# Kernel tuning notes

Hardware: AMD Instinct MI355X
Metric: run time of the kernel (lower is better)

The kernel has to match this reference:

```python
import jax, jax.numpy as jnp
import numpy as np

B, S, D, DOUT, E = 2, 2048, 1024, 1024, 8
DH = 4 * D  # expert hidden size


def setup_inputs() -> dict:
    key = jax.random.key(0)
    ks = jax.random.split(key, 7)
    sc = lambda *sh: 1.0 / np.sqrt(sh[-2]) if len(sh) >= 2 else 0.02
    return {
        "x": jax.random.normal(ks[0], (B, S, D), jnp.float32),
        "Wg": jax.random.normal(ks[1], (D, E), jnp.float32) / np.sqrt(D),
        "bg": jnp.zeros((E,), jnp.float32),
        "W1": jax.random.normal(ks[2], (E, D, DH), jnp.float32) / np.sqrt(D),
        "b1": jax.random.normal(ks[3], (E, DH), jnp.float32) * 0.02,
        "W2": jax.random.normal(ks[4], (E, DH, DOUT), jnp.float32) / np.sqrt(DH),
        "b2": jax.random.normal(ks[5], (E, DOUT), jnp.float32) * 0.02,
    }


def reference(x, Wg, bg, W1, b1, W2, b2):
    # x: [B, S, D] -> flatten tokens (chunking over seq in the original is
    # math-neutral: routing and expert MLP are per-token).
    Bb, Ss, Dd = x.shape
    xt = x.reshape(-1, Dd)                       # [T, D]
    # Gate: softmax then argmax (top-1 routing, output NOT scaled by gate prob)
    gates = jax.nn.softmax(xt @ Wg + bg, axis=-1)  # [T, E]
    sel = jnp.argmax(gates, axis=-1)               # [T]
    nE = W1.shape[0]
    out = jnp.zeros((xt.shape[0], W2.shape[-1]), x.dtype)
    # Grouped expert MLP expressed as masked dense loop over the small fixed
    # expert count (jit-friendly; a fused gather-grouped-GEMM-scatter kernel
    # is the optimization target).
    for e in range(nE):
        h = jax.nn.gelu(xt @ W1[e] + b1[e], approximate=False)  # [T, 4D]
        ye = h @ W2[e] + b2[e]                                  # [T, DOUT]
        out = jnp.where((sel == e)[:, None], ye, out)
    return out.reshape(Bb, Ss, -1)
```

## Files before the change

kernel.cpp:

```cpp
#include <hip/hip_runtime.h>
#include <hip/hip_bf16.h>
#include <math.h>

#define T_TOK 4096
#define DIM   1024
#define NEXP  8
#define DHID  4096
#define NDOUT 1024
#define BM    128
#define BN    128
#define BK    64
#define MAXTILES 40

typedef short bf16x8 __attribute__((ext_vector_type(8)));
typedef float f32x4 __attribute__((ext_vector_type(4)));

__device__ __forceinline__ unsigned short f2bf(float f) {
  unsigned u = __float_as_uint(f);
  u += 0x7fffu + ((u >> 16) & 1u);
  return (unsigned short)(u >> 16);
}
__device__ __forceinline__ unsigned pack2bf(float a, float b) {
  return (unsigned)f2bf(a) | ((unsigned)f2bf(b) << 16);
}
__device__ __forceinline__ void gl_lds16(const void* g, void* l) {
  __builtin_amdgcn_global_load_lds(
      (const __attribute__((address_space(1))) void*)g,
      (__attribute__((address_space(3))) void*)l, 16, 0, 0);
}

__global__ __launch_bounds__(256)
void gate_kernel(const float* __restrict__ x, const float* __restrict__ Wg,
                 const float* __restrict__ bg, int* __restrict__ sel) {
  int lane = threadIdx.x & 63;
  int wid  = threadIdx.x >> 6;
  int t = blockIdx.x * 4 + wid;
  if (t >= T_TOK) return;
  const float* xr = x + (size_t)t * DIM;
  double acc[NEXP];
#pragma unroll
  for (int e = 0; e < NEXP; e++) acc[e] = 0.0;
  for (int j = 0; j < DIM / 64; j++) {
    int d = lane + j * 64;
    float xv = xr[d];
    const float4* wr = reinterpret_cast<const float4*>(Wg + (size_t)d * NEXP);
    float4 w0 = wr[0], w1 = wr[1];
    acc[0] += (double)xv * (double)w0.x;
    acc[1] += (double)xv * (double)w0.y;
    acc[2] += (double)xv * (double)w0.z;
    acc[3] += (double)xv * (double)w0.w;
    acc[4] += (double)xv * (double)w1.x;
    acc[5] += (double)xv * (double)w1.y;
    acc[6] += (double)xv * (double)w1.z;
    acc[7] += (double)xv * (double)w1.w;
  }
#pragma unroll
  for (int off = 32; off >= 1; off >>= 1) {
#pragma unroll
    for (int e = 0; e < NEXP; e++) acc[e] += __shfl_down(acc[e], off);
  }
  if (lane == 0) {
    double best = acc[0] + (double)bg[0];
    int bi = 0;
#pragma unroll
    for (int e = 1; e < NEXP; e++) {
      double v = acc[e] + (double)bg[e];
      if (v > best) { best = v; bi = e; }
    }
    sel[t] = bi;
  }
}

__global__ void zero_kernel(int* __restrict__ counts) {
  if (threadIdx.x < NEXP) counts[threadIdx.x] = 0;
}

__global__ void hist_kernel(const int* __restrict__ sel, int* __restrict__ counts) {
  __shared__ int lc[NEXP];
  if (threadIdx.x < NEXP) lc[threadIdx.x] = 0;
  __syncthreads();
  int t = blockIdx.x * 256 + threadIdx.x;
  atomicAdd(&lc[sel[t]], 1);
  __syncthreads();
  if (threadIdx.x < NEXP) atomicAdd(&counts[threadIdx.x], lc[threadIdx.x]);
}

__global__ void plan_kernel(const int* __restrict__ counts, int* __restrict__ base,
                            int* __restrict__ cursor, int* __restrict__ tileExpert,
                            int* __restrict__ tilePos, int* __restrict__ tileRows,
                            int* __restrict__ ntiles) {
  if (threadIdx.x == 0) {
    int acc = 0, nt = 0;
    for (int e = 0; e < NEXP; e++) {
      base[e] = acc; cursor[e] = acc;
      int c = counts[e];
      for (int j = 0; j < c; j += BM) {
        tileExpert[nt] = e;
        tilePos[nt]    = acc + j;
        int rem = c - j;
        tileRows[nt]   = rem < BM ? rem : BM;
        nt++;
      }
      acc += c;
    }
    *ntiles = nt;
  }
}

__global__ void scatter_kernel(const int* __restrict__ sel, int* __restrict__ cursor,
                               int* __restrict__ list) {
  __shared__ int lcnt[NEXP];
  __shared__ int lbase[NEXP];
  int tid = threadIdx.x;
  if (tid < NEXP) lcnt[tid] = 0;
  __syncthreads();
  int t = blockIdx.x * 256 + tid;
  int e = sel[t];
  int lpos = atomicAdd(&lcnt[e], 1);
  __syncthreads();
  if (tid < NEXP) lbase[tid] = atomicAdd(&cursor[tid], lcnt[tid]);
  __syncthreads();
  list[lbase[e] + lpos] = t;
}

__global__ __launch_bounds__(256)
void convert_x_kernel(const float* __restrict__ x, unsigned short* __restrict__ xbf) {
  int i = (blockIdx.x * 256 + threadIdx.x) * 8;
  float4 a = *(const float4*)(x + i);
  float4 b = *(const float4*)(x + i + 4);
  uint4 o;
  o.x = pack2bf(a.x, a.y); o.y = pack2bf(a.z, a.w);
  o.z = pack2bf(b.x, b.y); o.w = pack2bf(b.z, b.w);
  *(uint4*)(xbf + i) = o;
}

__global__ __launch_bounds__(256)
void transpose_convert_kernel(const float* __restrict__ in, unsigned short* __restrict__ out,
                              int K, int N) {
  int nb = blockIdx.x, kb = blockIdx.y, e = blockIdx.z;
  const float* inp = in + (size_t)e * K * N;
  unsigned short* outp = out + (size_t)e * N * K;
  __shared__ unsigned short lds[64][72];
  int tx = threadIdx.x;
  int kloc = tx >> 4;
  int n4   = (tx & 15) << 2;
#pragma unroll
  for (int p = 0; p < 4; p++) {
    int k = p * 16 + kloc;
    float4 v = *(const float4*)(inp + (size_t)(kb * 64 + k) * N + nb * 64 + n4);
    lds[n4 + 0][k] = f2bf(v.x);
    lds[n4 + 1][k] = f2bf(v.y);
    lds[n4 + 2][k] = f2bf(v.z);
    lds[n4 + 3][k] = f2bf(v.w);
  }
  __syncthreads();
  int n  = tx >> 2;
  int kq = (tx & 3) << 4;
  uint4 a = *(const uint4*)&lds[n][kq];
  uint4 b = *(const uint4*)&lds[n][kq + 8];
  unsigned short* o = outp + (size_t)(nb * 64 + n) * K + kb * 64 + kq;
  *(uint4*)o = a;
  *(uint4*)(o + 8) = b;
}

__global__ __launch_bounds__(256)
void gemm1_kernel(const unsigned short* __restrict__ xbf, const unsigned short* __restrict__ W1T,
                  const float* __restrict__ b1, const int* __restrict__ list,
                  const int* __restrict__ tileExpert, const int* __restrict__ tilePos,
                  const int* __restrict__ tileRows, const int* __restrict__ ntiles,
                  unsigned short* __restrict__ Hc) {
  int tIdx = blockIdx.x;
  if (tIdx >= *ntiles) return;
  int e       = tileExpert[tIdx];
  int posBase = tilePos[tIdx];
  int rows    = tileRows[tIdx];
  int n0      = blockIdx.y * BN;

  __shared__ __align__(1024) unsigned char As[2][BM * 128];
  __shared__ __align__(1024) unsigned char Bs[2][BN * 128];

  const int tx   = threadIdx.x;
  const int lane = tx & 63;
  const int w    = tx >> 6;
  const int wm = w >> 1, wn = w & 1;
  const int u    = lane & 7;
  const int rsub = lane >> 3;
  const int px   = (u ^ rsub) << 4;

  const char* aSrc[4];
  const char* bSrc[4];
#pragma unroll
  for (int l = 0; l < 4; l++) {
    int r = w * 32 + l * 8 + rsub;
    int tok = list[posBase + (r < rows ? r : 0)];
    aSrc[l] = (const char*)xbf + ((size_t)tok * DIM) * 2 + px;
    bSrc[l] = (const char*)W1T + (((size_t)e * DHID + n0 + r) * DIM) * 2 + px;
  }

  f32x4 acc[4][4];
#pragma unroll
  for (int mf = 0; mf < 4; mf++)
#pragma unroll
    for (int nf = 0; nf < 4; nf++)
      acc[mf][nf] = f32x4{0.f, 0.f, 0.f, 0.f};

  const int NT = DIM / BK;
  auto stage = [&](int buf, int kt) {
    int kb = kt * 128;
#pragma unroll
    for (int l = 0; l < 4; l++) {
      gl_lds16(aSrc[l] + kb, &As[buf][(w * 32 + l * 8) * 128]);
      gl_lds16(bSrc[l] + kb, &Bs[buf][(w * 32 + l * 8) * 128]);
    }
  };
  auto compute = [&](int buf) {
#pragma unroll
    for (int ks = 0; ks < 2; ks++) {
      int kbl = ks * 64 + (lane >> 4) * 16;
      bf16x8 af[4], bv[4];
#pragma unroll
      for (int mf = 0; mf < 4; mf++) {
        int row = (wm << 6) + (mf << 4) + (lane & 15);
        af[mf] = *(const bf16x8*)&As[buf][row * 128 + (kbl ^ ((row & 7) << 4))];
      }
#pragma unroll
      for (int nf = 0; nf < 4; nf++) {
        int row = (wn << 6) + (nf << 4) + (lane & 15);
        bv[nf] = *(const bf16x8*)&Bs[buf][row * 128 + (kbl ^ ((row & 7) << 4))];
      }
#pragma unroll
      for (int mf = 0; mf < 4; mf++)
#pragma unroll
        for (int nf = 0; nf < 4; nf++)
          acc[mf][nf] = __builtin_amdgcn_mfma_f32_16x16x32_bf16(af[mf], bv[nf], acc[mf][nf], 0, 0, 0);
    }
  };

  stage(0, 0);
  __syncthreads();
  int cur = 0;
  for (int kt = 0; kt < NT; kt++) {
    if (kt + 1 < NT) stage(cur ^ 1, kt + 1);
    compute(cur);
    __syncthreads();
    cur ^= 1;
  }

  const float* b1e = b1 + (size_t)e * DHID;
#pragma unroll
  for (int nf = 0; nf < 4; nf++) {
    int col = n0 + (wn << 6) + (nf << 4) + (lane & 15);
    float bias = b1e[col];
#pragma unroll
    for (int mf = 0; mf < 4; mf++) {
#pragma unroll
      for (int j = 0; j < 4; j++) {
        int rloc = (wm << 6) + (mf << 4) + ((lane >> 4) << 2) + j;
        if (rloc < rows) {
          float h = acc[mf][nf][j] + bias;
          float g = 0.5f * h * (1.0f + erff(h * 0.70710678118654752f));
          Hc[(size_t)(posBase + rloc) * DHID + col] = f2bf(g);
        }
      }
    }
  }
}

__global__ __launch_bounds__(256)
void gemm2_kernel(const unsigned short* __restrict__ Hc, const unsigned short* __restrict__ W2T,
                  const float* __restrict__ b2, const int* __restrict__ list,
                  const int* __restrict__ tileExpert, const int* __restrict__ tilePos,
                  const int* __restrict__ tileRows, const int* __restrict__ ntiles,
                  float* __restrict__ out) {
  int tIdx = blockIdx.x;
  if (tIdx >= *ntiles) return;
  int e       = tileExpert[tIdx];
  int posBase = tilePos[tIdx];
  int rows    = tileRows[tIdx];
  int n0      = blockIdx.y * BN;

  __shared__ __align__(1024) unsigned char As[2][BM * 128];
  __shared__ __align__(1024) unsigned char Bs[2][BN * 128];

  const int tx   = threadIdx.x;
  const int lane = tx & 63;
  const int w    = tx >> 6;
  const int wm = w >> 1, wn = w & 1;
  const int u    = lane & 7;
  const int rsub = lane >> 3;
  const int px   = (u ^ rsub) << 4;

  const char* aSrc[4];
  const char* bSrc[4];
#pragma unroll
  for (int l = 0; l < 4; l++) {
    int r = w * 32 + l * 8 + rsub;
    int ar = posBase + (r < rows ? r : 0);
    aSrc[l] = (const char*)Hc + ((size_t)ar * DHID) * 2 + px;
    bSrc[l] = (const char*)W2T + (((size_t)e * NDOUT + n0 + r) * DHID) * 2 + px;
  }

  f32x4 acc[4][4];
#pragma unroll
  for (int mf = 0; mf < 4; mf++)
#pragma unroll
    for (int nf = 0; nf < 4; nf++)
      acc[mf][nf] = f32x4{0.f, 0.f, 0.f, 0.f};

  const int NT = DHID / BK;
  auto stage = [&](int buf, int kt) {
    int kb = kt * 128;
#pragma unroll
    for (int l = 0; l < 4; l++) {
      gl_lds16(aSrc[l] + kb, &As[buf][(w * 32 + l * 8) * 128]);
      gl_lds16(bSrc[l] + kb, &Bs[buf][(w * 32 + l * 8) * 128]);
    }
  };
  auto compute = [&](int buf) {
#pragma unroll
    for (int ks = 0; ks < 2; ks++) {
      int kbl = ks * 64 + (lane >> 4) * 16;
      bf16x8 af[4], bv[4];
#pragma unroll
      for (int mf = 0; mf < 4; mf++) {
        int row = (wm << 6) + (mf << 4) + (lane & 15);
        af[mf] = *(const bf16x8*)&As[buf][row * 128 + (kbl ^ ((row & 7) << 4))];
      }
#pragma unroll
      for (int nf = 0; nf < 4; nf++) {
        int row = (wn << 6) + (nf << 4) + (lane & 15);
        bv[nf] = *(const bf16x8*)&Bs[buf][row * 128 + (kbl ^ ((row & 7) << 4))];
      }
#pragma unroll
      for (int mf = 0; mf < 4; mf++)
#pragma unroll
        for (int nf = 0; nf < 4; nf++)
          acc[mf][nf] = __builtin_amdgcn_mfma_f32_16x16x32_bf16(af[mf], bv[nf], acc[mf][nf], 0, 0, 0);
    }
  };

  stage(0, 0);
  __syncthreads();
  int cur = 0;
  for (int kt = 0; kt < NT; kt++) {
    if (kt + 1 < NT) stage(cur ^ 1, kt + 1);
    compute(cur);
    __syncthreads();
    cur ^= 1;
  }

  const float* b2e = b2 + (size_t)e * NDOUT;
  int trow[4][4];
#pragma unroll
  for (int mf = 0; mf < 4; mf++)
#pragma unroll
    for (int j = 0; j < 4; j++) {
      int rloc = (wm << 6) + (mf << 4) + ((lane >> 4) << 2) + j;
      trow[mf][j] = (rloc < rows) ? list[posBase + rloc] : -1;
    }
#pragma unroll
  for (int nf = 0; nf < 4; nf++) {
    int col = n0 + (wn << 6) + (nf << 4) + (lane & 15);
    float bias = b2e[col];
#pragma unroll
    for (int mf = 0; mf < 4; mf++)
#pragma unroll
      for (int j = 0; j < 4; j++) {
        int t = trow[mf][j];
        if (t >= 0) out[(size_t)t * NDOUT + col] = acc[mf][nf][j] + bias;
      }
  }
}

extern "C" void kernel_launch(void* const* d_in, const int* in_sizes, int n_in,
                              void* d_out, int out_size, void* d_ws, size_t ws_size,
                              hipStream_t stream) {
  const float* x  = (const float*)d_in[0];
  const float* Wg = (const float*)d_in[1];
  const float* bg = (const float*)d_in[2];
  const float* W1 = (const float*)d_in[3];
  const float* b1 = (const float*)d_in[4];
  const float* W2 = (const float*)d_in[5];
  const float* b2 = (const float*)d_in[6];
  float* out = (float*)d_out;

  char* ws = (char*)d_ws;
  int* sel        = (int*)(ws);
  int* counts     = (int*)(ws + 16384);
  int* base       = (int*)(ws + 16448);
  int* cursor     = (int*)(ws + 16512);
  int* ntiles     = (int*)(ws + 16576);
  int* tileExpert = (int*)(ws + 16640);
  int* tilePos    = (int*)(ws + 16832);
  int* tileRows   = (int*)(ws + 17024);
  int* list       = (int*)(ws + 17408);

  unsigned short* xbf = (unsigned short*)(ws + (1ull << 20));
  unsigned short* Hc  = (unsigned short*)(ws + (16ull << 20));
  unsigned short* W1T = (unsigned short*)(ws + (48ull << 20));
  unsigned short* W2T = (unsigned short*)(ws + (112ull << 20));

  gate_kernel<<<T_TOK / 4, 256, 0, stream>>>(x, Wg, bg, sel);
  zero_kernel<<<1, 64, 0, stream>>>(counts);
  hist_kernel<<<T_TOK / 256, 256, 0, stream>>>(sel, counts);
  plan_kernel<<<1, 64, 0, stream>>>(counts, base, cursor, tileExpert, tilePos, tileRows, ntiles);
  scatter_kernel<<<T_TOK / 256, 256, 0, stream>>>(sel, cursor, list);

  convert_x_kernel<<<T_TOK * DIM / (256 * 8), 256, 0, stream>>>(x, xbf);
  transpose_convert_kernel<<<dim3(DHID / 64, DIM / 64, NEXP), 256, 0, stream>>>(W1, W1T, DIM, DHID);
  transpose_convert_kernel<<<dim3(NDOUT / 64, DHID / 64, NEXP), 256, 0, stream>>>(W2, W2T, DHID, NDOUT);

  gemm1_kernel<<<dim3(MAXTILES, DHID / BN), 256, 0, stream>>>(
      xbf, W1T, b1, list, tileExpert, tilePos, tileRows, ntiles, Hc);
  gemm2_kernel<<<dim3(MAXTILES, NDOUT / BN), 256, 0, stream>>>(
      Hc, W2T, b2, list, tileExpert, tilePos, tileRows, ntiles, out);
}
```

Measured before the change: 320.5 us.

## Use 256x256 tiles with staged pipelined MFMA schedule and split-K expert GEMM2

Both expert GEMMs move from 128x128 tiles with 256 threads to 256x256 tiles with 512 threads and a 128KB LDS double buffer. Each k-step is split into quarter-tile phases that interleave LDS reads, async global-to-LDS loads, explicit vmcnt waits, barriers and priority-raised MFMA bursts. The aim is more data reuse per tile and better overlap of memory traffic with matrix math. GEMM2 is split along K into two halves that write fp32 partials into workspace reused from the W1T region, and a new reduce kernel sums the halves and scatters rows back to token order. This adds an extra 32MB partial write and read plus one more launch, and with 256-row tiles the last tile of each expert carries more padding.

```diff
diff --git a/kernel.cpp b/kernel.cpp
--- a/kernel.cpp
+++ b/kernel.cpp
@@ -7,10 +7,7 @@
 #define NEXP  8
 #define DHID  4096
 #define NDOUT 1024
-#define BM    128
-#define BN    128
-#define BK    64
-#define MAXTILES 40
+#define MAXT2 24
 
 typedef short bf16x8 __attribute__((ext_vector_type(8)));
 typedef float f32x4 __attribute__((ext_vector_type(4)));
@@ -28,6 +25,8 @@
       (const __attribute__((address_space(1))) void*)g,
       (__attribute__((address_space(3))) void*)l, 16, 0, 0);
 }
+#define SBAR()  __builtin_amdgcn_s_barrier()
+#define SCHED() __builtin_amdgcn_sched_barrier(0)
 
 __global__ __launch_bounds__(256)
 void gate_kernel(const float* __restrict__ x, const float* __restrict__ Wg,
@@ -94,11 +93,11 @@
     for (int e = 0; e < NEXP; e++) {
       base[e] = acc; cursor[e] = acc;
       int c = counts[e];
-      for (int j = 0; j < c; j += BM) {
+      for (int j = 0; j < c; j += 256) {
         tileExpert[nt] = e;
         tilePos[nt]    = acc + j;
         int rem = c - j;
-        tileRows[nt]   = rem < BM ? rem : BM;
+        tileRows[nt]   = rem < 256 ? rem : 256;
         nt++;
       }
       acc += c;
@@ -163,213 +162,297 @@
   *(uint4*)(o + 8) = b;
 }
 
-__global__ __launch_bounds__(256)
+
+__global__ __launch_bounds__(512)
 void gemm1_kernel(const unsigned short* __restrict__ xbf, const unsigned short* __restrict__ W1T,
                   const float* __restrict__ b1, const int* __restrict__ list,
                   const int* __restrict__ tileExpert, const int* __restrict__ tilePos,
                   const int* __restrict__ tileRows, const int* __restrict__ ntiles,
                   unsigned short* __restrict__ Hc) {
-  int tIdx = blockIdx.x;
+  int tIdx = blockIdx.y;
   if (tIdx >= *ntiles) return;
-  int e       = tileExpert[tIdx];
-  int posBase = tilePos[tIdx];
-  int rows    = tileRows[tIdx];
-  int n0      = blockIdx.y * BN;
-
-  __shared__ __align__(1024) unsigned char As[2][BM * 128];
-  __shared__ __align__(1024) unsigned char Bs[2][BN * 128];
-
-  const int tx   = threadIdx.x;
-  const int lane = tx & 63;
-  const int w    = tx >> 6;
-  const int wm = w >> 1, wn = w & 1;
-  const int u    = lane & 7;
+  int e = tileExpert[tIdx], posBase = tilePos[tIdx], rows = tileRows[tIdx];
+  int n0 = blockIdx.x * 256;
+
+  __shared__ __align__(1024) char LDS[131072];
+
+  const int tx = threadIdx.x, lane = tx & 63, w = tx >> 6;
+  const int wm = w >> 2, wn = w & 3;
   const int rsub = lane >> 3;
-  const int px   = (u ^ rsub) << 4;
-
-  const char* aSrc[4];
-  const char* bSrc[4];
-#pragma unroll
-  for (int l = 0; l < 4; l++) {
-    int r = w * 32 + l * 8 + rsub;
-    int tok = list[posBase + (r < rows ? r : 0)];
-    aSrc[l] = (const char*)xbf + ((size_t)tok * DIM) * 2 + px;
-    bSrc[l] = (const char*)W1T + (((size_t)e * DHID + n0 + r) * DIM) * 2 + px;
-  }
-
-  f32x4 acc[4][4];
-#pragma unroll
-  for (int mf = 0; mf < 4; mf++)
-#pragma unroll
-    for (int nf = 0; nf < 4; nf++)
-      acc[mf][nf] = f32x4{0.f, 0.f, 0.f, 0.f};
-
-  const int NT = DIM / BK;
-  auto stage = [&](int buf, int kt) {
-    int kb = kt * 128;
-#pragma unroll
-    for (int l = 0; l < 4; l++) {
-      gl_lds16(aSrc[l] + kb, &As[buf][(w * 32 + l * 8) * 128]);
-      gl_lds16(bSrc[l] + kb, &Bs[buf][(w * 32 + l * 8) * 128]);
-    }
-  };
-  auto compute = [&](int buf) {
-#pragma unroll
-    for (int ks = 0; ks < 2; ks++) {
-      int kbl = ks * 64 + (lane >> 4) * 16;
-      bf16x8 af[4], bv[4];
-#pragma unroll
-      for (int mf = 0; mf < 4; mf++) {
-        int row = (wm << 6) + (mf << 4) + (lane & 15);
-        af[mf] = *(const bf16x8*)&As[buf][row * 128 + (kbl ^ ((row & 7) << 4))];
+  const int px = ((lane & 7) ^ rsub) << 4;
+
+  const char* aS[2][2];
+  const char* bS[2][2];
+#pragma unroll
+  for (int h = 0; h < 2; h++)
+#pragma unroll
+    for (int j = 0; j < 2; j++) {
+      int rl = w * 16 + j * 8 + rsub;
+      int ar = h * 128 + rl; if (ar >= rows) ar = rows - 1;
+      int tok = list[posBase + ar];
+      aS[h][j] = (const char*)xbf + (size_t)tok * (DIM * 2) + px;
+      bS[h][j] = (const char*)W1T + ((size_t)e * DHID + n0 + h * 128 + rl) * (DIM * 2) + px;
+    }
+
+  auto STAGE = [&](int buf, int isB, int half, int kt) {
+    char* base = &LDS[((buf * 2 + isB) * 2 + half) * 16384 + w * 2048];
+    const char* s0 = (isB ? bS[half][0] : aS[half][0]) + kt * 128;
+    const char* s1 = (isB ? bS[half][1] : aS[half][1]) + kt * 128;
+    gl_lds16(s0, base);
+    gl_lds16(s1, base + 1024);
+  };
+
+  const int koff0 = ((lane >> 4) * 16) ^ ((lane & 7) << 4);
+  const int koff1 = (64 + (lane >> 4) * 16) ^ ((lane & 7) << 4);
+
+  bf16x8 aF[4][2], bF0[2][2], bF1[2][2];
+  f32x4 acc[2][2][4][2];
+#pragma unroll
+  for (int qm = 0; qm < 2; qm++)
+#pragma unroll
+    for (int qn = 0; qn < 2; qn++)
+#pragma unroll
+      for (int mf = 0; mf < 4; mf++)
+#pragma unroll
+        for (int nf = 0; nf < 2; nf++)
+          acc[qm][qn][mf][nf] = f32x4{0.f, 0.f, 0.f, 0.f};
+
+  auto RDA = [&](int buf, int qm) {
+    const char* Ab = &LDS[((buf * 2 + 0) * 2 + qm) * 16384];
+#pragma unroll
+    for (int mf = 0; mf < 4; mf++) {
+      int ro = (wm * 64 + mf * 16 + (lane & 15)) * 128;
+      aF[mf][0] = *(const bf16x8*)(Ab + ro + koff0);
+      aF[mf][1] = *(const bf16x8*)(Ab + ro + koff1);
+    }
+  };
+  auto RDB = [&](int buf, int qn, bf16x8 (&bF)[2][2]) {
+    const char* Bb = &LDS[((buf * 2 + 1) * 2 + qn) * 16384];
+#pragma unroll
+    for (int nf = 0; nf < 2; nf++) {
+      int ro = (wn * 32 + nf * 16 + (lane & 15)) * 128;
+      bF[nf][0] = *(const bf16x8*)(Bb + ro + koff0);
+      bF[nf][1] = *(const bf16x8*)(Bb + ro + koff1);
+    }
+  };
+  auto MFMA16 = [&](int qm, int qn, bf16x8 (&bF)[2][2]) {
+    __builtin_amdgcn_s_setprio(1);
+#pragma unroll
+    for (int mf = 0; mf < 4; mf++)
+#pragma unroll
+      for (int nf = 0; nf < 2; nf++) {
+        acc[qm][qn][mf][nf] = __builtin_amdgcn_mfma_f32_16x16x32_bf16(aF[mf][0], bF[nf][0], acc[qm][qn][mf][nf], 0, 0, 0);
+        acc[qm][qn][mf][nf] = __builtin_amdgcn_mfma_f32_16x16x32_bf16(aF[mf][1], bF[nf][1], acc[qm][qn][mf][nf], 0, 0, 0);
       }
-#pragma unroll
-      for (int nf = 0; nf < 4; nf++) {
-        int row = (wn << 6) + (nf << 4) + (lane & 15);
-        bv[nf] = *(const bf16x8*)&Bs[buf][row * 128 + (kbl ^ ((row & 7) << 4))];
+    __builtin_amdgcn_s_setprio(0);
+  };
+
+  const int NTt = DIM / 64;
+  STAGE(0, 0, 0, 0); STAGE(0, 1, 0, 0); STAGE(0, 1, 1, 0); STAGE(0, 0, 1, 0);
+  STAGE(1, 0, 0, 1); STAGE(1, 1, 0, 1);
+  asm volatile("s_waitcnt vmcnt(4)" ::: "memory");
+  SCHED(); SBAR(); SCHED();
+
+  for (int T = 0; T < NTt; T++) {
+    int buf = T & 1, nbuf = buf ^ 1;
+    RDA(buf, 0); RDB(buf, 0, bF0);
+    if (T + 1 < NTt) STAGE(nbuf, 1, 1, T + 1);
+    SCHED(); SBAR(); SCHED();
+    MFMA16(0, 0, bF0);
+    SCHED(); SBAR(); SCHED();
+    RDB(buf, 1, bF1);
+    if (T + 1 < NTt) STAGE(nbuf, 0, 1, T + 1);
+    SCHED(); SBAR(); SCHED();
+    MFMA16(0, 1, bF1);
+    SCHED(); SBAR(); SCHED();
+    RDA(buf, 1);
+    if (T + 2 < NTt) STAGE(buf, 0, 0, T + 2);
+    SCHED(); SBAR(); SCHED();
+    MFMA16(1, 1, bF1);
+    SCHED(); SBAR(); SCHED();
+    if (T + 2 < NTt) {
+      STAGE(buf, 1, 0, T + 2);
+      asm volatile("s_waitcnt vmcnt(4)" ::: "memory");
+    } else if (T + 1 < NTt) {
+      asm volatile("s_waitcnt vmcnt(0)" ::: "memory");
+    }
+    SCHED(); SBAR(); SCHED();
+    MFMA16(1, 0, bF0);
+    SCHED(); SBAR(); SCHED();
+  }
+
+  const float* b1e = b1 + (size_t)e * DHID;
+#pragma unroll
+  for (int qm = 0; qm < 2; qm++)
+#pragma unroll
+    for (int qn = 0; qn < 2; qn++)
+#pragma unroll
+      for (int nf = 0; nf < 2; nf++) {
+        int col = n0 + qn * 128 + wn * 32 + nf * 16 + (lane & 15);
+        float bias = b1e[col];
+#pragma unroll
+        for (int mf = 0; mf < 4; mf++)
+#pragma unroll
+          for (int j = 0; j < 4; j++) {
+            int rloc = qm * 128 + wm * 64 + mf * 16 + ((lane >> 4) << 2) + j;
+            if (rloc < rows) {
+              float h = acc[qm][qn][mf][nf][j] + bias;
+              float g = 0.5f * h * (1.0f + erff(h * 0.70710678118654752f));
+              Hc[(size_t)(posBase + rloc) * DHID + col] = f2bf(g);
+            }
+          }
       }
+}
+
+__global__ __launch_bounds__(512)
+void gemm2_kernel(const unsigned short* __restrict__ Hc, const unsigned short* __restrict__ W2T,
+                  const float* __restrict__ b2, const int* __restrict__ tileExpert,
+                  const int* __restrict__ tilePos, const int* __restrict__ tileRows,
+                  const int* __restrict__ ntiles, float* __restrict__ Ppart) {
+  int tIdx = blockIdx.y;
+  if (tIdx >= *ntiles) return;
+  int e = tileExpert[tIdx], posBase = tilePos[tIdx], rows = tileRows[tIdx];
+  int n0 = blockIdx.x * 256;
+  int zs = blockIdx.z;
+  int kt0 = zs * 32;
+
+  __shared__ __align__(1024) char LDS[131072];
+
+  const int tx = threadIdx.x, lane = tx & 63, w = tx >> 6;
+  const int wm = w >> 2, wn = w & 3;
+  const int rsub = lane >> 3;
+  const int px = ((lane & 7) ^ rsub) << 4;
+
+  const char* aS[2][2];
+  const char* bS[2][2];
+#pragma unroll
+  for (int h = 0; h < 2; h++)
+#pragma unroll
+    for (int j = 0; j < 2; j++) {
+      int rl = w * 16 + j * 8 + rsub;
+      int ar = h * 128 + rl; if (ar >= rows) ar = rows - 1;
+      aS[h][j] = (const char*)Hc + (size_t)(posBase + ar) * (DHID * 2) + (size_t)kt0 * 128 + px;
+      bS[h][j] = (const char*)W2T + ((size_t)e * NDOUT + n0 + h * 128 + rl) * (DHID * 2) + (size_t)kt0 * 128 + px;
+    }
+
+  auto STAGE = [&](int buf, int isB, int half, int kt) {
+    char* base = &LDS[((buf * 2 + isB) * 2 + half) * 16384 + w * 2048];
+    const char* s0 = (isB ? bS[half][0] : aS[half][0]) + kt * 128;
+    const char* s1 = (isB ? bS[half][1] : aS[half][1]) + kt * 128;
+    gl_lds16(s0, base);
+    gl_lds16(s1, base + 1024);
+  };
+
+  const int koff0 = ((lane >> 4) * 16) ^ ((lane & 7) << 4);
+  const int koff1 = (64 + (lane >> 4) * 16) ^ ((lane & 7) << 4);
+
+  bf16x8 aF[4][2], bF0[2][2], bF1[2][2];
+  f32x4 acc[2][2][4][2];
+#pragma unroll
+  for (int qm = 0; qm < 2; qm++)
+#pragma unroll
+    for (int qn = 0; qn < 2; qn++)
 #pragma unroll
       for (int mf = 0; mf < 4; mf++)
 #pragma unroll
-        for (int nf = 0; nf < 4; nf++)
-          acc[mf][nf] = __builtin_amdgcn_mfma_f32_16x16x32_bf16(af[mf], bv[nf], acc[mf][nf], 0, 0, 0);
-    }
-  };
-
-  stage(0, 0);
-  __syncthreads();
-  int cur = 0;
-  for (int kt = 0; kt < NT; kt++) {
-    if (kt + 1 < NT) stage(cur ^ 1, kt + 1);
-    compute(cur);
-    __syncthreads();
-    cur ^= 1;
-  }
-
-  const float* b1e = b1 + (size_t)e * DHID;
-#pragma unroll
-  for (int nf = 0; nf < 4; nf++) {
-    int col = n0 + (wn << 6) + (nf << 4) + (lane & 15);
-    float bias = b1e[col];
+        for (int nf = 0; nf < 2; nf++)
+          acc[qm][qn][mf][nf] = f32x4{0.f, 0.f, 0.f, 0.f};
+
+  auto RDA = [&](int buf, int qm) {
+    const char* Ab = &LDS[((buf * 2 + 0) * 2 + qm) * 16384];
 #pragma unroll
     for (int mf = 0; mf < 4; mf++) {
-#pragma unroll
-      for (int j = 0; j < 4; j++) {
-        int rloc = (wm << 6) + (mf << 4) + ((lane >> 4) << 2) + j;
-        if (rloc < rows) {
-          float h = acc[mf][nf][j] + bias;
-          float g = 0.5f * h * (1.0f + erff(h * 0.70710678118654752f));
-          Hc[(size_t)(posBase + rloc) * DHID + col] = f2bf(g);
-        }
+      int ro = (wm * 64 + mf * 16 + (lane & 15)) * 128;
+      aF[mf][0] = *(const bf16x8*)(Ab + ro + koff0);
+      aF[mf][1] = *(const bf16x8*)(Ab + ro + koff1);
+    }
+  };
+  auto RDB = [&](int buf, int qn, bf16x8 (&bF)[2][2]) {
+    const char* Bb = &LDS[((buf * 2 + 1) * 2 + qn) * 16384];
+#pragma unroll
+    for (int nf = 0; nf < 2; nf++) {
+      int ro = (wn * 32 + nf * 16 + (lane & 15)) * 128;
+      bF[nf][0] = *(const bf16x8*)(Bb + ro + koff0);
+      bF[nf][1] = *(const bf16x8*)(Bb + ro + koff1);
+    }
+  };
+  auto MFMA16 = [&](int qm, int qn, bf16x8 (&bF)[2][2]) {
+    __builtin_amdgcn_s_setprio(1);
+#pragma unroll
+    for (int mf = 0; mf < 4; mf++)
+#pragma unroll
+      for (int nf = 0; nf < 2; nf++) {
+        acc[qm][qn][mf][nf] = __builtin_amdgcn_mfma_f32_16x16x32_bf16(aF[mf][0], bF[nf][0], acc[qm][qn][mf][nf], 0, 0, 0);
+        acc[qm][qn][mf][nf] = __builtin_amdgcn_mfma_f32_16x16x32_bf16(aF[mf][1], bF[nf][1], acc[qm][qn][mf][nf], 0, 0, 0);
       }
-    }
-  }
+    __builtin_amdgcn_s_setprio(0);
+  };
+
+  const int NTt = 32;
+  STAGE(0, 0, 0, 0); STAGE(0, 1, 0, 0); STAGE(0, 1, 1, 0); STAGE(0, 0, 1, 0);
+  STAGE(1, 0, 0, 1); STAGE(1, 1, 0, 1);
+  asm volatile("s_waitcnt vmcnt(4)" ::: "memory");
+  SCHED(); SBAR(); SCHED();
+
+  for (int T = 0; T < NTt; T++) {
+    int buf = T & 1, nbuf = buf ^ 1;
+    RDA(buf, 0); RDB(buf, 0, bF0);
+    if (T + 1 < NTt) STAGE(nbuf, 1, 1, T + 1);
+    SCHED(); SBAR(); SCHED();
+    MFMA16(0, 0, bF0);
+    SCHED(); SBAR(); SCHED();
+    RDB(buf, 1, bF1);
+    if (T + 1 < NTt) STAGE(nbuf, 0, 1, T + 1);
+    SCHED(); SBAR(); SCHED();
+    MFMA16(0, 1, bF1);
+    SCHED(); SBAR(); SCHED();
+    RDA(buf, 1);
+    if (T + 2 < NTt) STAGE(buf, 0, 0, T + 2);
+    SCHED(); SBAR(); SCHED();
+    MFMA16(1, 1, bF1);
+    SCHED(); SBAR(); SCHED();
+    if (T + 2 < NTt) {
+      STAGE(buf, 1, 0, T + 2);
+      asm volatile("s_waitcnt vmcnt(4)" ::: "memory");
+    } else if (T + 1 < NTt) {
+      asm volatile("s_waitcnt vmcnt(0)" ::: "memory");
+    }
+    SCHED(); SBAR(); SCHED();
+    MFMA16(1, 0, bF0);
+    SCHED(); SBAR(); SCHED();
+  }
+
+  const float* b2e = b2 + (size_t)e * NDOUT;
+  float* P = Ppart + (size_t)zs * T_TOK * NDOUT;
+#pragma unroll
+  for (int qm = 0; qm < 2; qm++)
+#pragma unroll
+    for (int qn = 0; qn < 2; qn++)
+#pragma unroll
+      for (int nf = 0; nf < 2; nf++) {
+        int col = n0 + qn * 128 + wn * 32 + nf * 16 + (lane & 15);
+        float bias = (zs == 0) ? b2e[col] : 0.f;
+#pragma unroll
+        for (int mf = 0; mf < 4; mf++)
+#pragma unroll
+          for (int j = 0; j < 4; j++) {
+            int rloc = qm * 128 + wm * 64 + mf * 16 + ((lane >> 4) << 2) + j;
+            if (rloc < rows)
+              P[(size_t)(posBase + rloc) * NDOUT + col] = acc[qm][qn][mf][nf][j] + bias;
+          }
+      }
 }
 
 __global__ __launch_bounds__(256)
-void gemm2_kernel(const unsigned short* __restrict__ Hc, const unsigned short* __restrict__ W2T,
-                  const float* __restrict__ b2, const int* __restrict__ list,
-                  const int* __restrict__ tileExpert, const int* __restrict__ tilePos,
-                  const int* __restrict__ tileRows, const int* __restrict__ ntiles,
-                  float* __restrict__ out) {
-  int tIdx = blockIdx.x;
-  if (tIdx >= *ntiles) return;
-  int e       = tileExpert[tIdx];
-  int posBase = tilePos[tIdx];
-  int rows    = tileRows[tIdx];
-  int n0      = blockIdx.y * BN;
-
-  __shared__ __align__(1024) unsigned char As[2][BM * 128];
-  __shared__ __align__(1024) unsigned char Bs[2][BN * 128];
-
-  const int tx   = threadIdx.x;
-  const int lane = tx & 63;
-  const int w    = tx >> 6;
-  const int wm = w >> 1, wn = w & 1;
-  const int u    = lane & 7;
-  const int rsub = lane >> 3;
-  const int px   = (u ^ rsub) << 4;
-
-  const char* aSrc[4];
-  const char* bSrc[4];
-#pragma unroll
-  for (int l = 0; l < 4; l++) {
-    int r = w * 32 + l * 8 + rsub;
-    int ar = posBase + (r < rows ? r : 0);
-    aSrc[l] = (const char*)Hc + ((size_t)ar * DHID) * 2 + px;
-    bSrc[l] = (const char*)W2T + (((size_t)e * NDOUT + n0 + r) * DHID) * 2 + px;
-  }
-
-  f32x4 acc[4][4];
-#pragma unroll
-  for (int mf = 0; mf < 4; mf++)
-#pragma unroll
-    for (int nf = 0; nf < 4; nf++)
-      acc[mf][nf] = f32x4{0.f, 0.f, 0.f, 0.f};
-
-  const int NT = DHID / BK;
-  auto stage = [&](int buf, int kt) {
-    int kb = kt * 128;
-#pragma unroll
-    for (int l = 0; l < 4; l++) {
-      gl_lds16(aSrc[l] + kb, &As[buf][(w * 32 + l * 8) * 128]);
-      gl_lds16(bSrc[l] + kb, &Bs[buf][(w * 32 + l * 8) * 128]);
-    }
-  };
-  auto compute = [&](int buf) {
-#pragma unroll
-    for (int ks = 0; ks < 2; ks++) {
-      int kbl = ks * 64 + (lane >> 4) * 16;
-      bf16x8 af[4], bv[4];
-#pragma unroll
-      for (int mf = 0; mf < 4; mf++) {
-        int row = (wm << 6) + (mf << 4) + (lane & 15);
-        af[mf] = *(const bf16x8*)&As[buf][row * 128 + (kbl ^ ((row & 7) << 4))];
-      }
-#pragma unroll
-      for (int nf = 0; nf < 4; nf++) {
-        int row = (wn << 6) + (nf << 4) + (lane & 15);
-        bv[nf] = *(const bf16x8*)&Bs[buf][row * 128 + (kbl ^ ((row & 7) << 4))];
-      }
-#pragma unroll
-      for (int mf = 0; mf < 4; mf++)
-#pragma unroll
-        for (int nf = 0; nf < 4; nf++)
-          acc[mf][nf] = __builtin_amdgcn_mfma_f32_16x16x32_bf16(af[mf], bv[nf], acc[mf][nf], 0, 0, 0);
-    }
-  };
-
-  stage(0, 0);
-  __syncthreads();
-  int cur = 0;
-  for (int kt = 0; kt < NT; kt++) {
-    if (kt + 1 < NT) stage(cur ^ 1, kt + 1);
-    compute(cur);
-    __syncthreads();
-    cur ^= 1;
-  }
-
-  const float* b2e = b2 + (size_t)e * NDOUT;
-  int trow[4][4];
-#pragma unroll
-  for (int mf = 0; mf < 4; mf++)
-#pragma unroll
-    for (int j = 0; j < 4; j++) {
-      int rloc = (wm << 6) + (mf << 4) + ((lane >> 4) << 2) + j;
-      trow[mf][j] = (rloc < rows) ? list[posBase + rloc] : -1;
-    }
-#pragma unroll
-  for (int nf = 0; nf < 4; nf++) {
-    int col = n0 + (wn << 6) + (nf << 4) + (lane & 15);
-    float bias = b2e[col];
-#pragma unroll
-    for (int mf = 0; mf < 4; mf++)
-#pragma unroll
-      for (int j = 0; j < 4; j++) {
-        int t = trow[mf][j];
-        if (t >= 0) out[(size_t)t * NDOUT + col] = acc[mf][nf][j] + bias;
-      }
-  }
+void reduce_kernel(const float* __restrict__ Ppart, const int* __restrict__ list,
+                   float* __restrict__ out) {
+  int pos = blockIdx.x;
+  int tok = list[pos];
+  int c = threadIdx.x * 4;
+  float4 a = *(const float4*)(Ppart + (size_t)pos * NDOUT + c);
+  float4 b = *(const float4*)(Ppart + (size_t)T_TOK * NDOUT + (size_t)pos * NDOUT + c);
+  float4 o; o.x = a.x + b.x; o.y = a.y + b.y; o.z = a.z + b.z; o.w = a.w + b.w;
+  *(float4*)(out + (size_t)tok * NDOUT + c) = o;
 }
 
 extern "C" void kernel_launch(void* const* d_in, const int* in_sizes, int n_in,
@@ -399,6 +482,7 @@
   unsigned short* Hc  = (unsigned short*)(ws + (16ull << 20));
   unsigned short* W1T = (unsigned short*)(ws + (48ull << 20));
   unsigned short* W2T = (unsigned short*)(ws + (112ull << 20));
+  float* Ppart        = (float*)(ws + (48ull << 20));
 
   gate_kernel<<<T_TOK / 4, 256, 0, stream>>>(x, Wg, bg, sel);
   zero_kernel<<<1, 64, 0, stream>>>(counts);
@@ -410,8 +494,9 @@
   transpose_convert_kernel<<<dim3(DHID / 64, DIM / 64, NEXP), 256, 0, stream>>>(W1, W1T, DIM, DHID);
   transpose_convert_kernel<<<dim3(NDOUT / 64, DHID / 64, NEXP), 256, 0, stream>>>(W2, W2T, DHID, NDOUT);
 
-  gemm1_kernel<<<dim3(MAXTILES, DHID / BN), 256, 0, stream>>>(
+  gemm1_kernel<<<dim3(DHID / 256, MAXT2), 512, 0, stream>>>(
       xbf, W1T, b1, list, tileExpert, tilePos, tileRows, ntiles, Hc);
-  gemm2_kernel<<<dim3(MAXTILES, NDOUT / BN), 256, 0, stream>>>(
-      Hc, W2T, b2, list, tileExpert, tilePos, tileRows, ntiles, out);
-}
+  gemm2_kernel<<<dim3(NDOUT / 256, MAXT2, 2), 512, 0, stream>>>(
+      Hc, W2T, b2, tileExpert, tilePos, tileRows, ntiles, Ppart);
+  reduce_kernel<<<T_TOK, 256, 0, stream>>>(Ppart, list, out);
+}
```

Result: faster. 289.5 us (-9.7%).

## Split-K the second expert GEMM, single-buffer LDS, and reorder grid axes

Applied to the files above, without the earlier changes.

The second grouped GEMM now splits its 4096-long K dimension in two along grid z. Each half writes fp32 partial results in compacted token order to a scratch buffer that reuses the W1T region. A new reduce kernel adds the two halves and scatters each row to its token position. Both GEMMs drop double-buffered LDS staging in favour of a single buffer synchronised twice per K step, which halves shared memory per block, and the grid axes are swapped so the N tile index varies fastest. The aim is more blocks in flight for the small-N second GEMM and higher occupancy, at the cost of an extra fp32 round trip through memory, an extra launch, and loss of load/compute overlap inside each block.

```diff
diff --git a/kernel.cpp b/kernel.cpp
--- a/kernel.cpp
+++ b/kernel.cpp
@@ -8,8 +8,6 @@
 #define DHID  4096
 #define NDOUT 1024
 #define BM    128
-#define BN    128
-#define BK    64
 #define MAXTILES 40
 
 typedef short bf16x8 __attribute__((ext_vector_type(8)));
@@ -163,38 +161,34 @@
   *(uint4*)(o + 8) = b;
 }
 
+
 __global__ __launch_bounds__(256)
 void gemm1_kernel(const unsigned short* __restrict__ xbf, const unsigned short* __restrict__ W1T,
                   const float* __restrict__ b1, const int* __restrict__ list,
                   const int* __restrict__ tileExpert, const int* __restrict__ tilePos,
                   const int* __restrict__ tileRows, const int* __restrict__ ntiles,
                   unsigned short* __restrict__ Hc) {
-  int tIdx = blockIdx.x;
+  int tIdx = blockIdx.y;
   if (tIdx >= *ntiles) return;
-  int e       = tileExpert[tIdx];
-  int posBase = tilePos[tIdx];
-  int rows    = tileRows[tIdx];
-  int n0      = blockIdx.y * BN;
-
-  __shared__ __align__(1024) unsigned char As[2][BM * 128];
-  __shared__ __align__(1024) unsigned char Bs[2][BN * 128];
-
-  const int tx   = threadIdx.x;
-  const int lane = tx & 63;
-  const int w    = tx >> 6;
+  int e = tileExpert[tIdx], posBase = tilePos[tIdx], rows = tileRows[tIdx];
+  int n0 = blockIdx.x * 128;
+
+  __shared__ __align__(1024) char As[128 * 128];
+  __shared__ __align__(1024) char Bs[128 * 128];
+
+  const int tx = threadIdx.x, lane = tx & 63, w = tx >> 6;
   const int wm = w >> 1, wn = w & 1;
-  const int u    = lane & 7;
   const int rsub = lane >> 3;
-  const int px   = (u ^ rsub) << 4;
-
-  const char* aSrc[4];
-  const char* bSrc[4];
-#pragma unroll
-  for (int l = 0; l < 4; l++) {
-    int r = w * 32 + l * 8 + rsub;
-    int tok = list[posBase + (r < rows ? r : 0)];
-    aSrc[l] = (const char*)xbf + ((size_t)tok * DIM) * 2 + px;
-    bSrc[l] = (const char*)W1T + (((size_t)e * DHID + n0 + r) * DIM) * 2 + px;
+  const int px = ((lane & 7) ^ rsub) << 4;
+
+  const char* aS[4];
+  const char* bS[4];
+#pragma unroll
+  for (int j = 0; j < 4; j++) {
+    int r = w * 32 + j * 8 + rsub;
+    int tok = list[posBase + (r < rows ? r : rows - 1)];
+    aS[j] = (const char*)xbf + (size_t)tok * (DIM * 2) + px;
+    bS[j] = (const char*)W1T + ((size_t)e * DHID + n0 + r) * (DIM * 2) + px;
   }
 
   f32x4 acc[4][4];
@@ -204,58 +198,44 @@
     for (int nf = 0; nf < 4; nf++)
       acc[mf][nf] = f32x4{0.f, 0.f, 0.f, 0.f};
 
-  const int NT = DIM / BK;
-  auto stage = [&](int buf, int kt) {
+  const int NT = DIM / 64;
+  for (int kt = 0; kt < NT; kt++) {
     int kb = kt * 128;
 #pragma unroll
-    for (int l = 0; l < 4; l++) {
-      gl_lds16(aSrc[l] + kb, &As[buf][(w * 32 + l * 8) * 128]);
-      gl_lds16(bSrc[l] + kb, &Bs[buf][(w * 32 + l * 8) * 128]);
-    }
-  };
-  auto compute = [&](int buf) {
+    for (int j = 0; j < 4; j++) {
+      gl_lds16(aS[j] + kb, &As[(w * 32 + j * 8) * 128]);
+      gl_lds16(bS[j] + kb, &Bs[(w * 32 + j * 8) * 128]);
+    }
+    __syncthreads();
 #pragma unroll
     for (int ks = 0; ks < 2; ks++) {
-      int kbl = ks * 64 + (lane >> 4) * 16;
-      bf16x8 af[4], bv[4];
-#pragma unroll
-      for (int mf = 0; mf < 4; mf++) {
-        int row = (wm << 6) + (mf << 4) + (lane & 15);
-        af[mf] = *(const bf16x8*)&As[buf][row * 128 + (kbl ^ ((row & 7) << 4))];
-      }
-#pragma unroll
-      for (int nf = 0; nf < 4; nf++) {
-        int row = (wn << 6) + (nf << 4) + (lane & 15);
-        bv[nf] = *(const bf16x8*)&Bs[buf][row * 128 + (kbl ^ ((row & 7) << 4))];
-      }
+      int koff = (ks * 64 + (lane >> 4) * 16) ^ ((lane & 7) << 4);
+      bf16x8 aF[4], bF[4];
 #pragma unroll
       for (int mf = 0; mf < 4; mf++)
+        aF[mf] = *(const bf16x8*)&As[(wm * 64 + mf * 16 + (lane & 15)) * 128 + koff];
+#pragma unroll
+      for (int nf = 0; nf < 4; nf++)
+        bF[nf] = *(const bf16x8*)&Bs[(wn * 64 + nf * 16 + (lane & 15)) * 128 + koff];
+#pragma unroll
+      for (int mf = 0; mf < 4; mf++)
 #pragma unroll
         for (int nf = 0; nf < 4; nf++)
-          acc[mf][nf] = __builtin_amdgcn_mfma_f32_16x16x32_bf16(af[mf], bv[nf], acc[mf][nf], 0, 0, 0);
-    }
-  };
-
-  stage(0, 0);
-  __syncthreads();
-  int cur = 0;
-  for (int kt = 0; kt < NT; kt++) {
-    if (kt + 1 < NT) stage(cur ^ 1, kt + 1);
-    compute(cur);
+          acc[mf][nf] = __builtin_amdgcn_mfma_f32_16x16x32_bf16(aF[mf], bF[nf], acc[mf][nf], 0, 0, 0);
+    }
     __syncthreads();
-    cur ^= 1;
   }
 
   const float* b1e = b1 + (size_t)e * DHID;
 #pragma unroll
   for (int nf = 0; nf < 4; nf++) {
-    int col = n0 + (wn << 6) + (nf << 4) + (lane & 15);
+    int col = n0 + wn * 64 + nf * 16 + (lane & 15);
     float bias = b1e[col];
 #pragma unroll
     for (int mf = 0; mf < 4; mf++) {
 #pragma unroll
       for (int j = 0; j < 4; j++) {
-        int rloc = (wm << 6) + (mf << 4) + ((lane >> 4) << 2) + j;
+        int rloc = wm * 64 + mf * 16 + ((lane >> 4) << 2) + j;
         if (rloc < rows) {
           float h = acc[mf][nf][j] + bias;
           float g = 0.5f * h * (1.0f + erff(h * 0.70710678118654752f));
@@ -268,36 +248,32 @@
 
 __global__ __launch_bounds__(256)
 void gemm2_kernel(const unsigned short* __restrict__ Hc, const unsigned short* __restrict__ W2T,
-                  const float* __restrict__ b2, const int* __restrict__ list,
-                  const int* __restrict__ tileExpert, const int* __restrict__ tilePos,
-                  const int* __restrict__ tileRows, const int* __restrict__ ntiles,
-                  float* __restrict__ out) {
-  int tIdx = blockIdx.x;
+                  const float* __restrict__ b2, const int* __restrict__ tileExpert,
+                  const int* __restrict__ tilePos, const int* __restrict__ tileRows,
+                  const int* __restrict__ ntiles, float* __restrict__ Ppart) {
+  int tIdx = blockIdx.y;
   if (tIdx >= *ntiles) return;
-  int e       = tileExpert[tIdx];
-  int posBase = tilePos[tIdx];
-  int rows    = tileRows[tIdx];
-  int n0      = blockIdx.y * BN;
-
-  __shared__ __align__(1024) unsigned char As[2][BM * 128];
-  __shared__ __align__(1024) unsigned char Bs[2][BN * 128];
-
-  const int tx   = threadIdx.x;
-  const int lane = tx & 63;
-  const int w    = tx >> 6;
+  int e = tileExpert[tIdx], posBase = tilePos[tIdx], rows = tileRows[tIdx];
+  int n0 = blockIdx.x * 128;
+  int zs = blockIdx.z;
+  size_t kbyte0 = (size_t)zs * 32 * 128;
+
+  __shared__ __align__(1024) char As[128 * 128];
+  __shared__ __align__(1024) char Bs[128 * 128];
+
+  const int tx = threadIdx.x, lane = tx & 63, w = tx >> 6;
   const int wm = w >> 1, wn = w & 1;
-  const int u    = lane & 7;
   const int rsub = lane >> 3;
-  const int px   = (u ^ rsub) << 4;
-
-  const char* aSrc[4];
-  const char* bSrc[4];
-#pragma unroll
-  for (int l = 0; l < 4; l++) {
-    int r = w * 32 + l * 8 + rsub;
-    int ar = posBase + (r < rows ? r : 0);
-    aSrc[l] = (const char*)Hc + ((size_t)ar * DHID) * 2 + px;
-    bSrc[l] = (const char*)W2T + (((size_t)e * NDOUT + n0 + r) * DHID) * 2 + px;
+  const int px = ((lane & 7) ^ rsub) << 4;
+
+  const char* aS[4];
+  const char* bS[4];
+#pragma unroll
+  for (int j = 0; j < 4; j++) {
+    int r = w * 32 + j * 8 + rsub;
+    int ar = posBase + (r < rows ? r : rows - 1);
+    aS[j] = (const char*)Hc + (size_t)ar * (DHID * 2) + kbyte0 + px;
+    bS[j] = (const char*)W2T + ((size_t)e * NDOUT + n0 + r) * (DHID * 2) + kbyte0 + px;
   }
 
   f32x4 acc[4][4];
@@ -307,69 +283,61 @@
     for (int nf = 0; nf < 4; nf++)
       acc[mf][nf] = f32x4{0.f, 0.f, 0.f, 0.f};
 
-  const int NT = DHID / BK;
-  auto stage = [&](int buf, int kt) {
+  const int NT = 32;
+  for (int kt = 0; kt < NT; kt++) {
     int kb = kt * 128;
 #pragma unroll
-    for (int l = 0; l < 4; l++) {
-      gl_lds16(aSrc[l] + kb, &As[buf][(w * 32 + l * 8) * 128]);
-      gl_lds16(bSrc[l] + kb, &Bs[buf][(w * 32 + l * 8) * 128]);
-    }
-  };
-  auto compute = [&](int buf) {
+    for (int j = 0; j < 4; j++) {
+      gl_lds16(aS[j] + kb, &As[(w * 32 + j * 8) * 128]);
+      gl_lds16(bS[j] + kb, &Bs[(w * 32 + j * 8) * 128]);
+    }
+    __syncthreads();
 #pragma unroll
     for (int ks = 0; ks < 2; ks++) {
-      int kbl = ks * 64 + (lane >> 4) * 16;
-      bf16x8 af[4], bv[4];
-#pragma unroll
-      for (int mf = 0; mf < 4; mf++) {
-        int row = (wm << 6) + (mf << 4) + (lane & 15);
-        af[mf] = *(const bf16x8*)&As[buf][row * 128 + (kbl ^ ((row & 7) << 4))];
+      int koff = (ks * 64 + (lane >> 4) * 16) ^ ((lane & 7) << 4);
+      bf16x8 aF[4], bF[4];
+#pragma unroll
+      for (int mf = 0; mf < 4; mf++)
+        aF[mf] = *(const bf16x8*)&As[(wm * 64 + mf * 16 + (lane & 15)) * 128 + koff];
+#pragma unroll
+      for (int nf = 0; nf < 4; nf++)
+        bF[nf] = *(const bf16x8*)&Bs[(wn * 64 + nf * 16 + (lane & 15)) * 128 + koff];
+#pragma unroll
+      for (int mf = 0; mf < 4; mf++)
+#pragma unroll
+        for (int nf = 0; nf < 4; nf++)
+          acc[mf][nf] = __builtin_amdgcn_mfma_f32_16x16x32_bf16(aF[mf], bF[nf], acc[mf][nf], 0, 0, 0);
+    }
+    __syncthreads();
+  }
+
+  const float* b2e = b2 + (size_t)e * NDOUT;
+  float* P = Ppart + (size_t)zs * T_TOK * NDOUT;
+#pragma unroll
+  for (int nf = 0; nf < 4; nf++) {
+    int col = n0 + wn * 64 + nf * 16 + (lane & 15);
+    float bias = (zs == 0) ? b2e[col] : 0.f;
+#pragma unroll
+    for (int mf = 0; mf < 4; mf++)
+#pragma unroll
+      for (int j = 0; j < 4; j++) {
+        int rloc = wm * 64 + mf * 16 + ((lane >> 4) << 2) + j;
+        if (rloc < rows)
+          P[(size_t)(posBase + rloc) * NDOUT + col] = acc[mf][nf][j] + bias;
       }
-#pragma unroll
-      for (int nf = 0; nf < 4; nf++) {
-        int row = (wn << 6) + (nf << 4) + (lane & 15);
-        bv[nf] = *(const bf16x8*)&Bs[buf][row * 128 + (kbl ^ ((row & 7) << 4))];
-      }
-#pragma unroll
-      for (int mf = 0; mf < 4; mf++)
-#pragma unroll
-        for (int nf = 0; nf < 4; nf++)
-          acc[mf][nf] = __builtin_amdgcn_mfma_f32_16x16x32_bf16(af[mf], bv[nf], acc[mf][nf], 0, 0, 0);
-    }
-  };
-
-  stage(0, 0);
-  __syncthreads();
-  int cur = 0;
-  for (int kt = 0; kt < NT; kt++) {
-    if (kt + 1 < NT) stage(cur ^ 1, kt + 1);
-    compute(cur);
-    __syncthreads();
-    cur ^= 1;
-  }
-
-  const float* b2e = b2 + (size_t)e * NDOUT;
-  int trow[4][4];
-#pragma unroll
-  for (int mf = 0; mf < 4; mf++)
-#pragma unroll
-    for (int j = 0; j < 4; j++) {
-      int rloc = (wm << 6) + (mf << 4) + ((lane >> 4) << 2) + j;
-      trow[mf][j] = (rloc < rows) ? list[posBase + rloc] : -1;
-    }
-#pragma unroll
-  for (int nf = 0; nf < 4; nf++) {
-    int col = n0 + (wn << 6) + (nf << 4) + (lane & 15);
-    float bias = b2e[col];
-#pragma unroll
-    for (int mf = 0; mf < 4; mf++)
-#pragma unroll
-      for (int j = 0; j < 4; j++) {
-        int t = trow[mf][j];
-        if (t >= 0) out[(size_t)t * NDOUT + col] = acc[mf][nf][j] + bias;
-      }
-  }
+  }
+}
+
+__global__ __launch_bounds__(256)
+void reduce_kernel(const float* __restrict__ Ppart, const int* __restrict__ list,
+                   float* __restrict__ out) {
+  int pos = blockIdx.x;
+  int tok = list[pos];
+  int c = threadIdx.x * 4;
+  float4 a = *(const float4*)(Ppart + (size_t)pos * NDOUT + c);
+  float4 b = *(const float4*)(Ppart + (size_t)T_TOK * NDOUT + (size_t)pos * NDOUT + c);
+  float4 o; o.x = a.x + b.x; o.y = a.y + b.y; o.z = a.z + b.z; o.w = a.w + b.w;
+  *(float4*)(out + (size_t)tok * NDOUT + c) = o;
 }
 
 extern "C" void kernel_launch(void* const* d_in, const int* in_sizes, int n_in,
@@ -399,6 +367,7 @@
   unsigned short* Hc  = (unsigned short*)(ws + (16ull << 20));
   unsigned short* W1T = (unsigned short*)(ws + (48ull << 20));
   unsigned short* W2T = (unsigned short*)(ws + (112ull << 20));
+  float* Ppart        = (float*)(ws + (48ull << 20));
 
   gate_kernel<<<T_TOK / 4, 256, 0, stream>>>(x, Wg, bg, sel);
   zero_kernel<<<1, 64, 0, stream>>>(counts);
@@ -410,8 +379,9 @@
   transpose_convert_kernel<<<dim3(DHID / 64, DIM / 64, NEXP), 256, 0, stream>>>(W1, W1T, DIM, DHID);
   transpose_convert_kernel<<<dim3(NDOUT / 64, DHID / 64, NEXP), 256, 0, stream>>>(W2, W2T, DHID, NDOUT);
 
-  gemm1_kernel<<<dim3(MAXTILES, DHID / BN), 256, 0, stream>>>(
+  gemm1_kernel<<<dim3(DHID / 128, MAXTILES), 256, 0, stream>>>(
       xbf, W1T, b1, list, tileExpert, tilePos, tileRows, ntiles, Hc);
-  gemm2_kernel<<<dim3(MAXTILES, NDOUT / BN), 256, 0, stream>>>(
-      Hc, W2T, b2, list, tileExpert, tilePos, tileRows, ntiles, out);
-}
+  gemm2_kernel<<<dim3(NDOUT / 128, MAXTILES, 2), 256, 0, stream>>>(
+      Hc, W2T, b2, tileExpert, tilePos, tileRows, ntiles, Ppart);
+  reduce_kernel<<<T_TOK, 256, 0, stream>>>(Ppart, list, out);
+}
```

Result: slower. 328.2 us (+2.4%).
